# Performance work log

Hardware: AMD Instinct MI355X
Metric: run time of the kernel (lower is better)

## Reference

```python
import jax, jax.numpy as jnp
import numpy as np

D_IN = 1024
D_SAE = 16384
K = 32
N = 8192

def setup_inputs() -> dict:
    key = jax.random.key(0)
    ks = jax.random.split(key, 3)
    x = jax.random.normal(ks[0], (N, D_IN), dtype=jnp.float32)
    W_enc = jax.random.normal(ks[1], (D_SAE, D_IN), dtype=jnp.float32) * 0.02
    W_dec = jax.random.normal(ks[2], (D_IN, D_SAE), dtype=jnp.float32) * 0.02
    b_pre = jnp.zeros((D_IN,), dtype=jnp.float32)
    b_dec = jnp.zeros((D_IN,), dtype=jnp.float32)
    return {"x": x, "b_pre": b_pre, "W_enc": W_enc, "W_dec": W_dec, "b_dec": b_dec}

def _topk_mask(z, k):
    # keep top-k values per row, zero elsewhere (scatter of topk vals)
    if k >= z.shape[-1]:
        return z
    vals, idx = jax.lax.top_k(z, k)            # [N, k]
    rows = jnp.arange(z.shape[0])[:, None]      # [N, 1]
    return jnp.zeros_like(z).at[rows, idx].set(vals)

def reference(x, b_pre, W_enc, W_dec, b_dec):
    x0 = x - b_pre                               # [N, d_in]
    z_pre = x0 @ W_enc.T                         # [N, d_sae]
    z = _topk_mask(z_pre, K)                     # [N, d_sae], k-sparse
    x_hat = z @ W_dec.T + b_dec + b_pre          # [N, d_in]
    return (x_hat, z, z_pre)
```

## Files before the change

### kernel.cpp

```cpp
#include <hip/hip_runtime.h>

#define D_IN   1024
#define D_SAE  16384
#define KTOP   32
#define NROWS  8192
#define KSPLIT 3072
#define LOSCALE 2048.0f
#define INV_LOSCALE 4.8828125e-4f
#define CAND_CAP 512

typedef _Float16 f16x8 __attribute__((ext_vector_type(8)));
typedef float    f32x4 __attribute__((ext_vector_type(4)));

__global__ __launch_bounds__(256) void split_xw(
    const float* __restrict__ x, const float* __restrict__ b_pre,
    const float* __restrict__ W_enc,
    _Float16* __restrict__ A2, _Float16* __restrict__ B2)
{
    const int b   = blockIdx.x;
    const int tid = threadIdx.x;
    const int k   = tid * 4;
    if (b < NROWS) {
        float4 v  = *(const float4*)(x + (size_t)b * D_IN + k);
        float4 bp = *(const float4*)(b_pre + k);
        v.x -= bp.x; v.y -= bp.y; v.z -= bp.z; v.w -= bp.w;
        _Float16 h[4], l[4];
        h[0] = (_Float16)v.x; l[0] = (_Float16)((v.x - (float)h[0]) * LOSCALE);
        h[1] = (_Float16)v.y; l[1] = (_Float16)((v.y - (float)h[1]) * LOSCALE);
        h[2] = (_Float16)v.z; l[2] = (_Float16)((v.z - (float)h[2]) * LOSCALE);
        h[3] = (_Float16)v.w; l[3] = (_Float16)((v.w - (float)h[3]) * LOSCALE);
        _Float16* row = A2 + (size_t)b * KSPLIT;
        *(ulong1*)(row + k)        = *(ulong1*)l;
        *(ulong1*)(row + 1024 + k) = *(ulong1*)h;
        *(ulong1*)(row + 2048 + k) = *(ulong1*)h;
    } else {
        const int s = b - NROWS;
        float4 v = *(const float4*)(W_enc + (size_t)s * D_IN + k);
        _Float16 h[4], l[4];
        h[0] = (_Float16)v.x; l[0] = (_Float16)((v.x - (float)h[0]) * LOSCALE);
        h[1] = (_Float16)v.y; l[1] = (_Float16)((v.y - (float)h[1]) * LOSCALE);
        h[2] = (_Float16)v.z; l[2] = (_Float16)((v.z - (float)h[2]) * LOSCALE);
        h[3] = (_Float16)v.w; l[3] = (_Float16)((v.w - (float)h[3]) * LOSCALE);
        _Float16* row = B2 + (size_t)s * KSPLIT;
        *(ulong1*)(row + k)        = *(ulong1*)h;
        *(ulong1*)(row + 1024 + k) = *(ulong1*)l;
        *(ulong1*)(row + 2048 + k) = *(ulong1*)h;
    }
}

__device__ __forceinline__ void gload_lds16(const void* g, void* lds) {
    __builtin_amdgcn_global_load_lds(
        (const __attribute__((address_space(1))) unsigned int*)g,
        (__attribute__((address_space(3))) unsigned int*)lds, 16, 0, 0);
}

__global__ __launch_bounds__(256, 2) void encode_mfma(
    const _Float16* __restrict__ A2, const _Float16* __restrict__ B2,
    float* __restrict__ z_pre)
{
    __shared__ _Float16 Asl[128 * 64];
    __shared__ _Float16 Bsl[128 * 64];

    const int tid  = threadIdx.x;
    const int wid  = tid >> 6;
    const int lane = tid & 63;
    const int wr   = wid >> 1;
    const int wc   = wid & 1;
    const int brow = blockIdx.y * 128;
    const int bcol = blockIdx.x * 128;

    const int srow = lane >> 3;
    const int scol = ((lane & 7) ^ srow) * 8;

    const int fr = lane & 15;
    const int fq = lane >> 4;
    const int slot0 = ((0 + fq) ^ (fr & 7)) * 8;
    const int slot1 = ((4 + fq) ^ (fr & 7)) * 8;

    f32x4 acc[4][4] = {};

    for (int k0 = 0; k0 < KSPLIT; k0 += 64) {
        if (k0 == 2048) {
#pragma unroll
            for (int m = 0; m < 4; ++m)
#pragma unroll
                for (int n = 0; n < 4; ++n) {
                    acc[m][n][0] *= INV_LOSCALE;
                    acc[m][n][1] *= INV_LOSCALE;
                    acc[m][n][2] *= INV_LOSCALE;
                    acc[m][n][3] *= INV_LOSCALE;
                }
        }
#pragma unroll
        for (int t = 0; t < 4; ++t) {
            const int rg = (wid * 4 + t) * 8 + srow;
            const char* ldsA = (const char*)Asl + (wid * 4 + t) * 1024;
            const char* ldsB = (const char*)Bsl + (wid * 4 + t) * 1024;
            gload_lds16(A2 + (size_t)(brow + rg) * KSPLIT + k0 + scol, (void*)ldsA);
            gload_lds16(B2 + (size_t)(bcol + rg) * KSPLIT + k0 + scol, (void*)ldsB);
        }
        __syncthreads();

#pragma unroll
        for (int kk = 0; kk < 2; ++kk) {
            const int slot = kk ? slot1 : slot0;
            f16x8 a[4], b[4];
#pragma unroll
            for (int m = 0; m < 4; ++m)
                a[m] = *(const f16x8*)&Asl[(wr * 64 + m * 16 + fr) * 64 + slot];
#pragma unroll
            for (int n = 0; n < 4; ++n)
                b[n] = *(const f16x8*)&Bsl[(wc * 64 + n * 16 + fr) * 64 + slot];
#pragma unroll
            for (int m = 0; m < 4; ++m)
#pragma unroll
                for (int n = 0; n < 4; ++n)
                    acc[m][n] = __builtin_amdgcn_mfma_f32_16x16x32_f16(a[m], b[n], acc[m][n], 0, 0, 0);
        }
        __syncthreads();
    }

#pragma unroll
    for (int m = 0; m < 4; ++m) {
        const int r0 = brow + wr * 64 + m * 16 + (lane >> 4) * 4;
#pragma unroll
        for (int n = 0; n < 4; ++n) {
            float* dst = z_pre + (size_t)r0 * D_SAE + bcol + wc * 64 + n * 16 + (lane & 15);
#pragma unroll
            for (int j = 0; j < 4; ++j)
                dst[(size_t)j * D_SAE] = acc[m][n][j];
        }
    }
}

__global__ __launch_bounds__(256, 2) void encode_gemm(
    const float* __restrict__ x, const float* __restrict__ b_pre,
    const float* __restrict__ W_enc, float* __restrict__ z_pre)
{
    __shared__ float As[16][132];
    __shared__ float Bs[16][132];
    const int tid = threadIdx.x;
    const int n0  = blockIdx.y * 128;
    const int s0  = blockIdx.x * 128;
    const int ty  = tid >> 4;
    const int tx  = tid & 15;
    const int r0  = tid >> 2;
    const int r1  = r0 + 64;
    const int kq  = (tid & 3) * 4;
    float acc[8][8];
#pragma unroll
    for (int i = 0; i < 8; ++i)
#pragma unroll
        for (int j = 0; j < 8; ++j) acc[i][j] = 0.0f;
    const float* xA = x     + (size_t)n0 * D_IN;
    const float* wB = W_enc + (size_t)s0 * D_IN;
    for (int k0 = 0; k0 < D_IN; k0 += 16) {
        float4 a0 = *(const float4*)(xA + (size_t)r0 * D_IN + k0 + kq);
        float4 a1 = *(const float4*)(xA + (size_t)r1 * D_IN + k0 + kq);
        float4 b0 = *(const float4*)(wB + (size_t)r0 * D_IN + k0 + kq);
        float4 b1 = *(const float4*)(wB + (size_t)r1 * D_IN + k0 + kq);
        float4 bp = *(const float4*)(b_pre + k0 + kq);
        a0.x -= bp.x; a0.y -= bp.y; a0.z -= bp.z; a0.w -= bp.w;
        a1.x -= bp.x; a1.y -= bp.y; a1.z -= bp.z; a1.w -= bp.w;
        __syncthreads();
        As[kq + 0][r0] = a0.x; As[kq + 1][r0] = a0.y; As[kq + 2][r0] = a0.z; As[kq + 3][r0] = a0.w;
        As[kq + 0][r1] = a1.x; As[kq + 1][r1] = a1.y; As[kq + 2][r1] = a1.z; As[kq + 3][r1] = a1.w;
        Bs[kq + 0][r0] = b0.x; Bs[kq + 1][r0] = b0.y; Bs[kq + 2][r0] = b0.z; Bs[kq + 3][r0] = b0.w;
        Bs[kq + 0][r1] = b1.x; Bs[kq + 1][r1] = b1.y; Bs[kq + 2][r1] = b1.z; Bs[kq + 3][r1] = b1.w;
        __syncthreads();
#pragma unroll
        for (int kk = 0; kk < 16; ++kk) {
            float4 av0 = *(const float4*)&As[kk][ty * 8];
            float4 av1 = *(const float4*)&As[kk][ty * 8 + 4];
            float4 bv0 = *(const float4*)&Bs[kk][tx * 8];
            float4 bv1 = *(const float4*)&Bs[kk][tx * 8 + 4];
            float a[8] = {av0.x, av0.y, av0.z, av0.w, av1.x, av1.y, av1.z, av1.w};
            float b[8] = {bv0.x, bv0.y, bv0.z, bv0.w, bv1.x, bv1.y, bv1.z, bv1.w};
#pragma unroll
            for (int i = 0; i < 8; ++i)
#pragma unroll
                for (int j = 0; j < 8; ++j)
                    acc[i][j] = fmaf(a[i], b[j], acc[i][j]);
        }
    }
#pragma unroll
    for (int i = 0; i < 8; ++i) {
        float* dst = z_pre + (size_t)(n0 + ty * 8 + i) * D_SAE + s0 + tx * 8;
        *(float4*)(dst)     = make_float4(acc[i][0], acc[i][1], acc[i][2], acc[i][3]);
        *(float4*)(dst + 4) = make_float4(acc[i][4], acc[i][5], acc[i][6], acc[i][7]);
    }
}

__device__ __forceinline__ unsigned int f2su(float f) {
    unsigned int b = __float_as_uint(f);
    return (b & 0x80000000u) ? ~b : (b | 0x80000000u);
}
__device__ __forceinline__ float su2f(unsigned int su) {
    unsigned int fb = (su & 0x80000000u) ? (su & 0x7fffffffu) : ~su;
    return __uint_as_float(fb);
}

__global__ __launch_bounds__(256) void topk_select4(
    const float* __restrict__ z_pre, float* __restrict__ z,
    int* __restrict__ out_idx, float* __restrict__ out_val)
{
    __shared__ unsigned int hist[4096];
    __shared__ unsigned int cmax[256];
    __shared__ unsigned int sb[256];
    __shared__ unsigned int cand_su[CAND_CAP];
    __shared__ int          cand_idx[CAND_CAP];
    __shared__ unsigned int cand_cnt;
    __shared__ int          hot[256];
    __shared__ unsigned int nhot;
    __shared__ int   sel_list[KTOP];
    __shared__ float sel_val[KTOP];
    __shared__ int s_bin, s_gt;
    __shared__ int cidx[KTOP];
    __shared__ float cvals[KTOP];
    __shared__ unsigned int outcnt;
    __shared__ unsigned int wcw[4];

    const int row  = blockIdx.x;
    const int tid  = threadIdx.x;
    const int wid  = tid >> 6;
    const int lane = tid & 63;
    const float* src = z_pre + (size_t)row * D_SAE;

    const int shifts[3] = {20, 8, 0};
    const int nbits_[3] = {12, 12, 8};

    cmax[tid] = 0u;
    if (tid == 0) { cand_cnt = 0u; outcnt = 0u; nhot = 0u; }

    unsigned int prefix = 0u, pmask = 0u;
    int need = KTOP;
    int shiftF = 0;

    for (int level = 0; level < 3; ++level) {
        const int shift = shifts[level];
        const unsigned int nb = 1u << nbits_[level];
        for (int i = tid; i < (int)nb; i += 256) hist[i] = 0u;
        __syncthreads();

        for (int it = 0; it < 16; ++it) {
            const int i4 = (it * 256 + tid) * 4;
            float4 v = *(const float4*)(src + i4);
            unsigned int mx = 0u;
#pragma unroll
            for (int e = 0; e < 4; ++e) {
                unsigned int su = f2su((&v.x)[e]);
                if ((su & pmask) == prefix)
                    atomicAdd(&hist[(su >> shift) & (nb - 1u)], 1u);
                mx = su > mx ? su : mx;
            }
            if (level == 0) atomicMax(&cmax[i4 >> 6], mx);
        }
        __syncthreads();

        const int bpt = (int)(nb >> 8);
        unsigned int lsum = 0u;
        for (int j = 0; j < bpt; ++j) lsum += hist[tid * bpt + j];
        sb[tid] = lsum;
        __syncthreads();
        for (int off = 1; off < 256; off <<= 1) {
            unsigned int v = (tid + off < 256) ? sb[tid + off] : 0u;
            __syncthreads();
            sb[tid] += v;
            __syncthreads();
        }
        {
            unsigned int ge = sb[tid];
            unsigned int gt = (tid < 255) ? sb[tid + 1] : 0u;
            if ((int)ge >= need && (int)gt < need) {
                unsigned int run = gt;
                for (int j = bpt - 1; j >= 0; --j) {
                    unsigned int c = hist[tid * bpt + j];
                    if ((int)(run + c) >= need) { s_bin = tid * bpt + j; s_gt = (int)run; break; }
                    run += c;
                }
            }
        }
        __syncthreads();
        const int b  = s_bin;
        const int gt = s_gt;
        const int cntb = (int)hist[b];
        __syncthreads();

        need  -= gt;
        prefix |= ((unsigned int)b) << shift;
        pmask  |= (nb - 1u) << shift;

        if (cntb <= CAND_CAP) { shiftF = shift; break; }
        if (level == 2)       { shiftF = 0;     break; }
    }
    const unsigned int hb = prefix >> shiftF;

    if (cmax[tid] >= prefix) {
        unsigned int p = atomicAdd(&nhot, 1u);
        hot[p] = tid;
    }
    __syncthreads();

    const int nh = (int)nhot;
    for (int h = wid; h < nh; h += 4) {
        const int c = hot[h];
        const int i = c * 64 + lane;
        const float f = src[i];
        const unsigned int su = f2su(f);
        const unsigned int cls = su >> shiftF;
        if (cls > hb) {
            z[(size_t)row * D_SAE + i] = f;
            unsigned int p = atomicAdd(&outcnt, 1u);
            if (p < (unsigned)KTOP) { cidx[p] = i; cvals[p] = f; }
        } else if (cls == hb) {
            unsigned int p = atomicAdd(&cand_cnt, 1u);
            if (p < (unsigned)CAND_CAP) { cand_su[p] = su; cand_idx[p] = i; }
        }
    }
    __syncthreads();

    if (cand_cnt <= (unsigned)CAND_CAP) {
        const int cnt = (int)cand_cnt;
        for (int c = tid; c < cnt; c += 256) {
            const unsigned int s = cand_su[c];
            const int id = cand_idx[c];
            int r = 0;
            for (int j = 0; j < cnt; ++j) {
                const unsigned int sj = cand_su[j];
                r += (sj > s) || (sj == s && cand_idx[j] < id);
            }
            if (r < need) { sel_list[r] = id; sel_val[r] = su2f(s); }
        }
        __syncthreads();
    } else {
        int cum = 0;
        for (int seg = 0; seg < 64; ++seg) {
            const int i = seg * 256 + tid;
            const bool m = (f2su(src[i]) == prefix);
            const unsigned long long bm = __ballot(m);
            if (lane == 0) wcw[wid] = (unsigned int)__popcll(bm);
            __syncthreads();
            int base = cum;
            for (int w = 0; w < wid; ++w) base += (int)wcw[w];
            const int r = base + (int)__popcll(bm & ((1ull << lane) - 1ull));
            if (m && r < need) { sel_list[r] = i; sel_val[r] = su2f(prefix); }
            cum += (int)(wcw[0] + wcw[1] + wcw[2] + wcw[3]);
            __syncthreads();
            if (cum >= need) break;
        }
        __syncthreads();
    }

    if (tid < need) {
        const int id = sel_list[tid];
        const float fv = sel_val[tid];
        z[(size_t)row * D_SAE + id] = fv;
        unsigned int p = atomicAdd(&outcnt, 1u);
        cidx[p] = id; cvals[p] = fv;
    }
    __syncthreads();

    if (out_idx != nullptr && tid < KTOP) {
        const int id = cidx[tid];
        const float vv = cvals[tid];
        int r = 0;
        for (int j = 0; j < KTOP; ++j) r += (cidx[j] < id);
        out_idx[row * KTOP + r] = id;
        out_val[row * KTOP + r] = vv;
    }
}

__global__ __launch_bounds__(256) void transpose_wdec(
    const float* __restrict__ in, float* __restrict__ out)
{
    __shared__ float tile[32][33];
    const int tid = threadIdx.x;
    const int lx = tid & 31, ly = tid >> 5;
    const int j0 = blockIdx.x * 32;
    const int d0 = blockIdx.y * 32;
#pragma unroll
    for (int r = 0; r < 4; ++r) {
        int d = d0 + ly + r * 8;
        tile[ly + r * 8][lx] = in[(size_t)d * D_SAE + j0 + lx];
    }
    __syncthreads();
#pragma unroll
    for (int r = 0; r < 4; ++r) {
        int j = j0 + ly + r * 8;
        out[(size_t)j * D_IN + d0 + lx] = tile[lx][ly + r * 8];
    }
}

__global__ __launch_bounds__(256) void decode_fast(
    const float* __restrict__ WdT, const int* __restrict__ idx,
    const float* __restrict__ val, const float* __restrict__ b_pre,
    const float* __restrict__ b_dec, float* __restrict__ x_hat)
{
    __shared__ int   sj[KTOP];
    __shared__ float sv[KTOP];
    const int row = blockIdx.x, tid = threadIdx.x;
    if (tid < KTOP) { sj[tid] = idx[row * KTOP + tid]; sv[tid] = val[row * KTOP + tid]; }
    __syncthreads();
    const int d = tid * 4;
    float4 bd = *(const float4*)(b_dec + d);
    float4 bp = *(const float4*)(b_pre + d);
    float4 acc = make_float4(bd.x + bp.x, bd.y + bp.y, bd.z + bp.z, bd.w + bp.w);
#pragma unroll
    for (int j = 0; j < KTOP; ++j) {
        const float v = sv[j];
        const float4 w = *(const float4*)(WdT + (size_t)sj[j] * D_IN + d);
        acc.x = fmaf(v, w.x, acc.x); acc.y = fmaf(v, w.y, acc.y);
        acc.z = fmaf(v, w.z, acc.z); acc.w = fmaf(v, w.w, acc.w);
    }
    *(float4*)(x_hat + (size_t)row * D_IN + d) = acc;
}

__global__ __launch_bounds__(256) void decode_slow(
    const float* __restrict__ W_dec, const float* __restrict__ z,
    const float* __restrict__ b_pre, const float* __restrict__ b_dec,
    float* __restrict__ x_hat)
{
    __shared__ int   sj[64];
    __shared__ float sv[64];
    __shared__ unsigned int cnt;
    __shared__ int s_m;
    const int row = blockIdx.x, tid = threadIdx.x;
    if (tid == 0) cnt = 0u;
    __syncthreads();
    const float* zr = z + (size_t)row * D_SAE;
    for (int i = tid; i < D_SAE; i += 256) {
        float v = zr[i];
        if (v != 0.0f) { unsigned p = atomicAdd(&cnt, 1u); if (p < 64u) { sj[p] = i; sv[p] = v; } }
    }
    __syncthreads();
    if (tid == 0) {
        int m = (int)(cnt < 64u ? cnt : 64u);
        for (int a = 1; a < m; ++a) {
            int vi = sj[a]; float vv = sv[a]; int b = a - 1;
            while (b >= 0 && sj[b] > vi) { sj[b + 1] = sj[b]; sv[b + 1] = sv[b]; --b; }
            sj[b + 1] = vi; sv[b + 1] = vv;
        }
        s_m = m;
    }
    __syncthreads();
    const int m = s_m;
    const int d = tid * 4;
    float4 bd = *(const float4*)(b_dec + d);
    float4 bp = *(const float4*)(b_pre + d);
    float4 acc = make_float4(bd.x + bp.x, bd.y + bp.y, bd.z + bp.z, bd.w + bp.w);
    for (int j = 0; j < m; ++j) {
        float v = sv[j];
        size_t c = (size_t)sj[j];
        acc.x = fmaf(v, W_dec[(size_t)(d + 0) * D_SAE + c], acc.x);
        acc.y = fmaf(v, W_dec[(size_t)(d + 1) * D_SAE + c], acc.y);
        acc.z = fmaf(v, W_dec[(size_t)(d + 2) * D_SAE + c], acc.z);
        acc.w = fmaf(v, W_dec[(size_t)(d + 3) * D_SAE + c], acc.w);
    }
    *(float4*)(x_hat + (size_t)row * D_IN + d) = acc;
}

extern "C" void kernel_launch(void* const* d_in, const int* in_sizes, int n_in,
                              void* d_out, int out_size, void* d_ws, size_t ws_size,
                              hipStream_t stream)
{
    const float* x     = (const float*)d_in[0];
    const float* b_pre = (const float*)d_in[1];
    const float* W_enc = (const float*)d_in[2];
    const float* W_dec = (const float*)d_in[3];
    const float* b_dec = (const float*)d_in[4];

    float* x_hat = (float*)d_out;
    float* z     = x_hat + (size_t)NROWS * D_IN;
    float* z_pre = z + (size_t)NROWS * D_SAE;

    const size_t wdt_bytes  = (size_t)D_SAE * D_IN * sizeof(float);
    const size_t list_bytes = (size_t)NROWS * KTOP * (sizeof(int) + sizeof(float));
    const size_t a2_bytes   = (size_t)NROWS * KSPLIT * sizeof(_Float16);
    const size_t b2_bytes   = (size_t)D_SAE * KSPLIT * sizeof(_Float16);

    char* p = (char*)d_ws;
    float*    WdT  = (float*)p;            p += wdt_bytes;
    int*      idxl = (int*)p;              p += (size_t)NROWS * KTOP * sizeof(int);
    float*    vall = (float*)p;            p += (size_t)NROWS * KTOP * sizeof(float);
    _Float16* A2   = (_Float16*)p;         p += a2_bytes;
    _Float16* B2   = (_Float16*)p;

    const bool fast = (ws_size >= wdt_bytes + list_bytes);
    const bool mfma = (ws_size >= wdt_bytes + list_bytes + a2_bytes + b2_bytes);

    hipMemsetAsync(z, 0, (size_t)NROWS * D_SAE * sizeof(float), stream);

    if (mfma) {
        split_xw<<<NROWS + D_SAE, 256, 0, stream>>>(x, b_pre, W_enc, A2, B2);
        encode_mfma<<<dim3(D_SAE / 128, NROWS / 128), 256, 0, stream>>>(A2, B2, z_pre);
    } else {
        encode_gemm<<<dim3(D_SAE / 128, NROWS / 128), 256, 0, stream>>>(x, b_pre, W_enc, z_pre);
    }

    if (fast) {
        transpose_wdec<<<dim3(D_SAE / 32, D_IN / 32), 256, 0, stream>>>(W_dec, WdT);
        topk_select4<<<NROWS, 256, 0, stream>>>(z_pre, z, idxl, vall);
        decode_fast<<<NROWS, 256, 0, stream>>>(WdT, idxl, vall, b_pre, b_dec, x_hat);
    } else {
        topk_select4<<<NROWS, 256, 0, stream>>>(z_pre, z, nullptr, nullptr);
        decode_slow<<<NROWS, 256, 0, stream>>>(W_dec, z, b_pre, b_dec, x_hat);
    }
}
```

Baseline: 1.302 ms.

## Fuse chunk maxima into GEMM epilogue, simplify top-k, store transposed W_dec as bf16

The encode MFMA epilogue now computes per-row maxima over 64-column chunks and writes them to a workspace array. A new top-k kernel uses them to find the 32nd-largest chunk max as a threshold, scans only the hot chunks, and ranks the candidates directly. This removes the multi-level histogram passes over the full z_pre row. Separately, the transposed W_dec copy is stored as bf16, halving decode gather traffic at the cost of reduced decode precision.

```diff
diff --git a/kernel.cpp b/kernel.cpp
--- a/kernel.cpp
+++ b/kernel.cpp
@@ -8,9 +8,23 @@
 #define LOSCALE 2048.0f
 #define INV_LOSCALE 4.8828125e-4f
 #define CAND_CAP 512
+#define NCHUNK 256
 
 typedef _Float16 f16x8 __attribute__((ext_vector_type(8)));
 typedef float    f32x4 __attribute__((ext_vector_type(4)));
+
+__device__ __forceinline__ unsigned int f2su(float f) {
+    unsigned int b = __float_as_uint(f);
+    return (b & 0x80000000u) ? ~b : (b | 0x80000000u);
+}
+__device__ __forceinline__ float su2f(unsigned int su) {
+    unsigned int fb = (su & 0x80000000u) ? (su & 0x7fffffffu) : ~su;
+    return __uint_as_float(fb);
+}
+__device__ __forceinline__ unsigned short f2bf(float f) {
+    unsigned int u = __float_as_uint(f);
+    return (unsigned short)((u + 0x7fffu + ((u >> 16) & 1u)) >> 16);
+}
 
 __global__ __launch_bounds__(256) void split_xw(
     const float* __restrict__ x, const float* __restrict__ b_pre,
@@ -56,7 +70,7 @@
 
 __global__ __launch_bounds__(256, 2) void encode_mfma(
     const _Float16* __restrict__ A2, const _Float16* __restrict__ B2,
-    float* __restrict__ z_pre)
+    float* __restrict__ z_pre, unsigned int* __restrict__ cmax_g)
 {
     __shared__ _Float16 Asl[128 * 64];
     __shared__ _Float16 Bsl[128 * 64];
@@ -122,13 +136,36 @@
 
 #pragma unroll
     for (int m = 0; m < 4; ++m) {
-        const int r0 = brow + wr * 64 + m * 16 + (lane >> 4) * 4;
+        const int r0 = brow + wr * 64 + m * 16 + fq * 4;
 #pragma unroll
         for (int n = 0; n < 4; ++n) {
-            float* dst = z_pre + (size_t)r0 * D_SAE + bcol + wc * 64 + n * 16 + (lane & 15);
+            float* dst = z_pre + (size_t)r0 * D_SAE + bcol + wc * 64 + n * 16 + fr;
 #pragma unroll
             for (int j = 0; j < 4; ++j)
                 dst[(size_t)j * D_SAE] = acc[m][n][j];
+        }
+    }
+
+    const int chunk = (bcol >> 6) + wc;
+#pragma unroll
+    for (int m = 0; m < 4; ++m) {
+        float v[4];
+#pragma unroll
+        for (int j = 0; j < 4; ++j)
+            v[j] = fmaxf(fmaxf(acc[m][0][j], acc[m][1][j]),
+                         fmaxf(acc[m][2][j], acc[m][3][j]));
+#pragma unroll
+        for (int mask = 1; mask < 16; mask <<= 1) {
+#pragma unroll
+            for (int j = 0; j < 4; ++j)
+                v[j] = fmaxf(v[j], __shfl_xor(v[j], mask));
+        }
+        if (fr == 0) {
+#pragma unroll
+            for (int j = 0; j < 4; ++j) {
+                const int row = brow + wr * 64 + m * 16 + fq * 4 + j;
+                cmax_g[(size_t)row * NCHUNK + chunk] = f2su(v[j]);
+            }
         }
     }
 }
@@ -191,18 +228,124 @@
     }
 }
 
-__device__ __forceinline__ unsigned int f2su(float f) {
-    unsigned int b = __float_as_uint(f);
-    return (b & 0x80000000u) ? ~b : (b | 0x80000000u);
-}
-__device__ __forceinline__ float su2f(unsigned int su) {
-    unsigned int fb = (su & 0x80000000u) ? (su & 0x7fffffffu) : ~su;
-    return __uint_as_float(fb);
+__global__ __launch_bounds__(256) void cmax_from_zpre(
+    const float* __restrict__ z_pre, unsigned int* __restrict__ cmax_g)
+{
+    const int row = blockIdx.x;
+    const int c   = threadIdx.x;
+    const float* src = z_pre + (size_t)row * D_SAE + c * 64;
+    unsigned int mx = 0u;
+    for (int e = 0; e < 64; ++e) mx = max(mx, f2su(src[e]));
+    cmax_g[(size_t)row * NCHUNK + c] = mx;
+}
+
+__global__ __launch_bounds__(256) void topk_select5(
+    const float* __restrict__ z_pre, const unsigned int* __restrict__ cmax_g,
+    float* __restrict__ z, int* __restrict__ out_idx, float* __restrict__ out_val)
+{
+    __shared__ unsigned int cm[NCHUNK];
+    __shared__ unsigned int s_sm32;
+    __shared__ int          hot[NCHUNK];
+    __shared__ unsigned int nhot;
+    __shared__ unsigned int cand_su[CAND_CAP];
+    __shared__ int          cand_idx[CAND_CAP];
+    __shared__ unsigned int cand_cnt;
+    __shared__ int   sidx[KTOP];
+    __shared__ float sval[KTOP];
+    __shared__ unsigned int bsu[256];
+    __shared__ int          bidx[256];
+
+    const int row  = blockIdx.x;
+    const int tid  = threadIdx.x;
+    const int wid  = tid >> 6;
+    const int lane = tid & 63;
+    const float* src = z_pre + (size_t)row * D_SAE;
+
+    if (tid == 0) { nhot = 0u; cand_cnt = 0u; }
+    cm[tid] = cmax_g[(size_t)row * NCHUNK + tid];
+    __syncthreads();
+
+    {
+        const unsigned int v = cm[tid];
+        int r = 0;
+        for (int j = 0; j < NCHUNK; ++j)
+            r += (cm[j] > v) || (cm[j] == v && j < tid);
+        if (r == KTOP - 1) s_sm32 = v;
+    }
+    __syncthreads();
+    const unsigned int sm32 = s_sm32;
+
+    if (cm[tid] >= sm32) { unsigned int p = atomicAdd(&nhot, 1u); hot[p] = tid; }
+    __syncthreads();
+
+    const int nh = (int)nhot;
+    for (int h = wid; h < nh; h += 4) {
+        const int i = hot[h] * 64 + lane;
+        const unsigned int su = f2su(src[i]);
+        if (su >= sm32) {
+            unsigned int p = atomicAdd(&cand_cnt, 1u);
+            if (p < (unsigned)CAND_CAP) { cand_su[p] = su; cand_idx[p] = i; }
+        }
+    }
+    __syncthreads();
+
+    if (cand_cnt <= (unsigned)CAND_CAP) {
+        const int cnt = (int)cand_cnt;
+        for (int c = tid; c < cnt; c += 256) {
+            const unsigned int s = cand_su[c];
+            const int id = cand_idx[c];
+            int r = 0;
+            for (int j = 0; j < cnt; ++j) {
+                const unsigned int sj = cand_su[j];
+                r += (sj > s) || (sj == s && cand_idx[j] < id);
+            }
+            if (r < KTOP) { sidx[r] = id; sval[r] = su2f(s); }
+        }
+        __syncthreads();
+    } else {
+        unsigned int last_su = 0xFFFFFFFFu; int last_idx = -1;
+        for (int r = 0; r < KTOP; ++r) {
+            unsigned int mysu = 0u; int myidx = 0x7FFFFFFF;
+            for (int i = tid; i < D_SAE; i += 256) {
+                const unsigned int su = f2su(src[i]);
+                const bool after = (su < last_su) || (su == last_su && i > last_idx);
+                if (after && (su > mysu || (su == mysu && i < myidx))) {
+                    mysu = su; myidx = i;
+                }
+            }
+            bsu[tid] = mysu; bidx[tid] = myidx;
+            __syncthreads();
+            if (tid == 0) {
+                unsigned int bs = 0u; int bi = 0x7FFFFFFF;
+                for (int j = 0; j < 256; ++j) {
+                    if (bsu[j] > bs || (bsu[j] == bs && bidx[j] < bi)) {
+                        bs = bsu[j]; bi = bidx[j];
+                    }
+                }
+                sidx[r] = bi; sval[r] = su2f(bs);
+                bsu[0] = bs; bidx[0] = bi;
+            }
+            __syncthreads();
+            last_su = bsu[0]; last_idx = bidx[0];
+            __syncthreads();
+        }
+    }
+
+    if (tid < KTOP) {
+        const int id = sidx[tid];
+        const float fv = sval[tid];
+        z[(size_t)row * D_SAE + id] = fv;
+        if (out_idx != nullptr) {
+            int r = 0;
+            for (int j = 0; j < KTOP; ++j) r += (sidx[j] < id);
+            out_idx[row * KTOP + r] = id;
+            out_val[row * KTOP + r] = fv;
+        }
+    }
 }
 
 __global__ __launch_bounds__(256) void topk_select4(
-    const float* __restrict__ z_pre, float* __restrict__ z,
-    int* __restrict__ out_idx, float* __restrict__ out_val)
+    const float* __restrict__ z_pre, float* __restrict__ z)
 {
     __shared__ unsigned int hist[4096];
     __shared__ unsigned int cmax[256];
@@ -215,9 +358,6 @@
     __shared__ int   sel_list[KTOP];
     __shared__ float sel_val[KTOP];
     __shared__ int s_bin, s_gt;
-    __shared__ int cidx[KTOP];
-    __shared__ float cvals[KTOP];
-    __shared__ unsigned int outcnt;
     __shared__ unsigned int wcw[4];
 
     const int row  = blockIdx.x;
@@ -230,7 +370,7 @@
     const int nbits_[3] = {12, 12, 8};
 
     cmax[tid] = 0u;
-    if (tid == 0) { cand_cnt = 0u; outcnt = 0u; nhot = 0u; }
+    if (tid == 0) { cand_cnt = 0u; nhot = 0u; }
 
     unsigned int prefix = 0u, pmask = 0u;
     int need = KTOP;
@@ -241,7 +381,6 @@
         const unsigned int nb = 1u << nbits_[level];
         for (int i = tid; i < (int)nb; i += 256) hist[i] = 0u;
         __syncthreads();
-
         for (int it = 0; it < 16; ++it) {
             const int i4 = (it * 256 + tid) * 4;
             float4 v = *(const float4*)(src + i4);
@@ -256,7 +395,6 @@
             if (level == 0) atomicMax(&cmax[i4 >> 6], mx);
         }
         __syncthreads();
-
         const int bpt = (int)(nb >> 8);
         unsigned int lsum = 0u;
         for (int j = 0; j < bpt; ++j) lsum += hist[tid * bpt + j];
@@ -281,37 +419,30 @@
             }
         }
         __syncthreads();
-        const int b  = s_bin;
-        const int gt = s_gt;
-        const int cntb = (int)hist[b];
-        __syncthreads();
-
-        need  -= gt;
+        const int b = s_bin; const int gt = s_gt; const int cntb = (int)hist[b];
+        __syncthreads();
+        need -= gt;
         prefix |= ((unsigned int)b) << shift;
         pmask  |= (nb - 1u) << shift;
-
         if (cntb <= CAND_CAP) { shiftF = shift; break; }
         if (level == 2)       { shiftF = 0;     break; }
     }
     const unsigned int hb = prefix >> shiftF;
 
-    if (cmax[tid] >= prefix) {
-        unsigned int p = atomicAdd(&nhot, 1u);
-        hot[p] = tid;
-    }
-    __syncthreads();
-
+    if (cmax[tid] >= prefix) { unsigned int p = atomicAdd(&nhot, 1u); hot[p] = tid; }
+    __syncthreads();
+
+    __shared__ unsigned int outcnt;
+    if (tid == 0) outcnt = 0u;
+    __syncthreads();
     const int nh = (int)nhot;
     for (int h = wid; h < nh; h += 4) {
-        const int c = hot[h];
-        const int i = c * 64 + lane;
+        const int i = hot[h] * 64 + lane;
         const float f = src[i];
         const unsigned int su = f2su(f);
         const unsigned int cls = su >> shiftF;
         if (cls > hb) {
             z[(size_t)row * D_SAE + i] = f;
-            unsigned int p = atomicAdd(&outcnt, 1u);
-            if (p < (unsigned)KTOP) { cidx[p] = i; cvals[p] = f; }
         } else if (cls == hb) {
             unsigned int p = atomicAdd(&cand_cnt, 1u);
             if (p < (unsigned)CAND_CAP) { cand_su[p] = su; cand_idx[p] = i; }
@@ -350,28 +481,11 @@
         }
         __syncthreads();
     }
-
-    if (tid < need) {
-        const int id = sel_list[tid];
-        const float fv = sel_val[tid];
-        z[(size_t)row * D_SAE + id] = fv;
-        unsigned int p = atomicAdd(&outcnt, 1u);
-        cidx[p] = id; cvals[p] = fv;
-    }
-    __syncthreads();
-
-    if (out_idx != nullptr && tid < KTOP) {
-        const int id = cidx[tid];
-        const float vv = cvals[tid];
-        int r = 0;
-        for (int j = 0; j < KTOP; ++j) r += (cidx[j] < id);
-        out_idx[row * KTOP + r] = id;
-        out_val[row * KTOP + r] = vv;
-    }
-}
-
-__global__ __launch_bounds__(256) void transpose_wdec(
-    const float* __restrict__ in, float* __restrict__ out)
+    if (tid < need) z[(size_t)row * D_SAE + sel_list[tid]] = sel_val[tid];
+}
+
+__global__ __launch_bounds__(256) void transpose_wdec_bf16(
+    const float* __restrict__ in, unsigned short* __restrict__ out)
 {
     __shared__ float tile[32][33];
     const int tid = threadIdx.x;
@@ -387,12 +501,12 @@
 #pragma unroll
     for (int r = 0; r < 4; ++r) {
         int j = j0 + ly + r * 8;
-        out[(size_t)j * D_IN + d0 + lx] = tile[lx][ly + r * 8];
-    }
-}
-
-__global__ __launch_bounds__(256) void decode_fast(
-    const float* __restrict__ WdT, const int* __restrict__ idx,
+        out[(size_t)j * D_IN + d0 + lx] = f2bf(tile[lx][ly + r * 8]);
+    }
+}
+
+__global__ __launch_bounds__(256) void decode_fast_bf16(
+    const unsigned short* __restrict__ WdT, const int* __restrict__ idx,
     const float* __restrict__ val, const float* __restrict__ b_pre,
     const float* __restrict__ b_dec, float* __restrict__ x_hat)
 {
@@ -408,9 +522,11 @@
 #pragma unroll
     for (int j = 0; j < KTOP; ++j) {
         const float v = sv[j];
-        const float4 w = *(const float4*)(WdT + (size_t)sj[j] * D_IN + d);
-        acc.x = fmaf(v, w.x, acc.x); acc.y = fmaf(v, w.y, acc.y);
-        acc.z = fmaf(v, w.z, acc.z); acc.w = fmaf(v, w.w, acc.w);
+        const ushort4 w = *(const ushort4*)(WdT + (size_t)sj[j] * D_IN + d);
+        acc.x = fmaf(v, __uint_as_float((unsigned int)w.x << 16), acc.x);
+        acc.y = fmaf(v, __uint_as_float((unsigned int)w.y << 16), acc.y);
+        acc.z = fmaf(v, __uint_as_float((unsigned int)w.z << 16), acc.z);
+        acc.w = fmaf(v, __uint_as_float((unsigned int)w.w << 16), acc.w);
     }
     *(float4*)(x_hat + (size_t)row * D_IN + d) = acc;
 }
@@ -473,36 +589,39 @@
     float* z     = x_hat + (size_t)NROWS * D_IN;
     float* z_pre = z + (size_t)NROWS * D_SAE;
 
-    const size_t wdt_bytes  = (size_t)D_SAE * D_IN * sizeof(float);
+    const size_t wdt_bytes  = (size_t)D_SAE * D_IN * sizeof(unsigned short);
     const size_t list_bytes = (size_t)NROWS * KTOP * (sizeof(int) + sizeof(float));
+    const size_t cmax_bytes = (size_t)NROWS * NCHUNK * sizeof(unsigned int);
     const size_t a2_bytes   = (size_t)NROWS * KSPLIT * sizeof(_Float16);
     const size_t b2_bytes   = (size_t)D_SAE * KSPLIT * sizeof(_Float16);
 
     char* p = (char*)d_ws;
-    float*    WdT  = (float*)p;            p += wdt_bytes;
-    int*      idxl = (int*)p;              p += (size_t)NROWS * KTOP * sizeof(int);
-    float*    vall = (float*)p;            p += (size_t)NROWS * KTOP * sizeof(float);
-    _Float16* A2   = (_Float16*)p;         p += a2_bytes;
-    _Float16* B2   = (_Float16*)p;
-
-    const bool fast = (ws_size >= wdt_bytes + list_bytes);
-    const bool mfma = (ws_size >= wdt_bytes + list_bytes + a2_bytes + b2_bytes);
+    unsigned short* WdT  = (unsigned short*)p;  p += wdt_bytes;
+    int*            idxl = (int*)p;             p += (size_t)NROWS * KTOP * sizeof(int);
+    float*          vall = (float*)p;           p += (size_t)NROWS * KTOP * sizeof(float);
+    unsigned int*   cmax = (unsigned int*)p;    p += cmax_bytes;
+    _Float16*       A2   = (_Float16*)p;        p += a2_bytes;
+    _Float16*       B2   = (_Float16*)p;
+
+    const bool fast = (ws_size >= wdt_bytes + list_bytes + cmax_bytes);
+    const bool mfma = (ws_size >= wdt_bytes + list_bytes + cmax_bytes + a2_bytes + b2_bytes);
 
     hipMemsetAsync(z, 0, (size_t)NROWS * D_SAE * sizeof(float), stream);
 
     if (mfma) {
         split_xw<<<NROWS + D_SAE, 256, 0, stream>>>(x, b_pre, W_enc, A2, B2);
-        encode_mfma<<<dim3(D_SAE / 128, NROWS / 128), 256, 0, stream>>>(A2, B2, z_pre);
+        encode_mfma<<<dim3(D_SAE / 128, NROWS / 128), 256, 0, stream>>>(A2, B2, z_pre, cmax);
     } else {
         encode_gemm<<<dim3(D_SAE / 128, NROWS / 128), 256, 0, stream>>>(x, b_pre, W_enc, z_pre);
+        if (fast) cmax_from_zpre<<<NROWS, 256, 0, stream>>>(z_pre, cmax);
     }
 
     if (fast) {
-        transpose_wdec<<<dim3(D_SAE / 32, D_IN / 32), 256, 0, stream>>>(W_dec, WdT);
-        topk_select4<<<NROWS, 256, 0, stream>>>(z_pre, z, idxl, vall);
-        decode_fast<<<NROWS, 256, 0, stream>>>(WdT, idxl, vall, b_pre, b_dec, x_hat);
+        transpose_wdec_bf16<<<dim3(D_SAE / 32, D_IN / 32), 256, 0, stream>>>(W_dec, WdT);
+        topk_select5<<<NROWS, 256, 0, stream>>>(z_pre, cmax, z, idxl, vall);
+        decode_fast_bf16<<<NROWS, 256, 0, stream>>>(WdT, idxl, vall, b_pre, b_dec, x_hat);
     } else {
-        topk_select4<<<NROWS, 256, 0, stream>>>(z_pre, z, nullptr, nullptr);
+        topk_select4<<<NROWS, 256, 0, stream>>>(z_pre, z);
         decode_slow<<<NROWS, 256, 0, stream>>>(W_dec, z, b_pre, b_dec, x_hat);
     }
 }
```

Result: faster. 1.135 ms (-12.8%).
